# Kernel optimization log

Measured on AMD Instinct MI355X. Metric: run time of the kernel, lower is better.

## Reference

```python
import jax, jax.numpy as jnp
import numpy as np

H, HD, D = 16, 64, 1024
SCALE = HD ** -0.5
TEMP = 1.0
EPS = 1e-5

def setup_inputs() -> dict:
    key = jax.random.key(0)
    ks = jax.random.split(key, 10)
    B, N = 2, 2048
    lim = 1.0 / np.sqrt(D)
    def lin(k, out_d, in_d):
        k1, k2 = jax.random.split(k)
        W = jax.random.uniform(k1, (out_d, in_d), jnp.float32, -lim, lim)
        b = jax.random.uniform(k2, (out_d,), jnp.float32, -lim, lim)
        return W, b
    Wq, bq = lin(ks[0], H * HD, D)
    Wk, bk = lin(ks[1], H * HD, D)
    Wv, bv = lin(ks[2], H * HD, D)
    Wo, bo = lin(ks[3], D, H * HD)
    return {
        "x": jax.random.normal(ks[4], (B, N, D), jnp.float32),
        "adaptive_scale": jnp.ones((H,), jnp.float32),
        "Wq": Wq, "bq": bq, "Wk": Wk, "bk": bk, "Wv": Wv, "bv": bv,
        "Wo": Wo, "bo": bo,
        "gamma": jnp.ones((D,), jnp.float32),
        "beta": jnp.zeros((D,), jnp.float32),
    }

def reference(x, adaptive_scale, Wq, bq, Wk, bk, Wv, bv, Wo, bo, gamma, beta):
    B, N, _ = x.shape
    # self-attention: context = x
    Q = (x @ Wq.T + bq).reshape(B, N, H, HD)
    K = (x @ Wk.T + bk).reshape(B, N, H, HD)
    V = (x @ Wv.T + bv).reshape(B, N, H, HD)
    # per-head adaptive scale folded into scores (matches naive QK^T * scale / temp)
    scores = jnp.einsum('bnhd,bmhd->bhnm', Q, K)
    scores = scores * (SCALE * adaptive_scale)[None, :, None, None] / TEMP
    w = jax.nn.softmax(scores, axis=-1)  # [B,H,N,N]
    attn = jnp.einsum('bhnm,bmhd->bnhd', w, V).reshape(B, N, H * HD)
    y = x + (attn @ Wo.T + bo)
    mu = jnp.mean(y, axis=-1, keepdims=True)
    var = jnp.var(y, axis=-1, keepdims=True)
    return (y - mu) / jnp.sqrt(var + EPS) * gamma + beta
```

## Files before the change

### kernel.cpp

```cpp
#include <hip/hip_runtime.h>
#include <hip/hip_bf16.h>

using bf16 = __hip_bfloat16;
typedef __attribute__((ext_vector_type(8))) short short8;
typedef __attribute__((ext_vector_type(4))) float f32x4;

#define MFMA16(a, b, c) __builtin_amdgcn_mfma_f32_16x16x32_bf16((a), (b), (c), 0, 0, 0)

__device__ inline void async16(bf16* lds, const bf16* g) {
  __builtin_amdgcn_global_load_lds(
      (const __attribute__((address_space(1))) void*)g,
      (__attribute__((address_space(3))) void*)lds, 16, 0, 0);
}

__global__ __launch_bounds__(256) void cvt_all(
    const float* __restrict__ x,  const float* __restrict__ Wq,
    const float* __restrict__ Wk, const float* __restrict__ Wv,
    const float* __restrict__ Wo,
    bf16* __restrict__ xb, bf16* __restrict__ Wqb, bf16* __restrict__ Wkb,
    bf16* __restrict__ Wvb, bf16* __restrict__ Wob) {
  int i = blockIdx.x * 256 + threadIdx.x;
  const float* s; bf16* d; int off;
  if (i < 1048576)      { s = x;  d = xb;  off = i; }
  else if (i < 1310720) { s = Wq; d = Wqb; off = i - 1048576; }
  else if (i < 1572864) { s = Wk; d = Wkb; off = i - 1310720; }
  else if (i < 1835008) { s = Wv; d = Wvb; off = i - 1572864; }
  else                  { s = Wo; d = Wob; off = i - 1835008; }
  float4 v = ((const float4*)s)[off];
  struct __align__(8) B4 { bf16 a, b, c, d; };
  B4 o{__float2bfloat16(v.x), __float2bfloat16(v.y),
       __float2bfloat16(v.z), __float2bfloat16(v.w)};
  *(B4*)&d[(size_t)off * 4] = o;
}

__global__ __launch_bounds__(256) void gemm_qkv(
    const bf16* __restrict__ A,
    const bf16* __restrict__ Wq, const bf16* __restrict__ Wk, const bf16* __restrict__ Wv,
    const float* __restrict__ bq, const float* __restrict__ bk, const float* __restrict__ bv,
    const float* __restrict__ asc,
    bf16* __restrict__ Qb, bf16* __restrict__ Kb, bf16* __restrict__ Vtb) {
  __shared__ __align__(16) bf16 As[128 * 32];
  __shared__ __align__(16) bf16 Bs[128 * 32];

  const int tid = threadIdx.x;
  const int lane = tid & 63;
  const int w = tid >> 6;
  const int m0 = blockIdx.x * 128;
  const int region = blockIdx.y >> 3;
  const int n0loc = (blockIdx.y & 7) * 128;
  const int wm = (w >> 1) * 64;
  const int wn = (w & 1) * 64;
  const int rq = lane & 15;
  const int quad = lane >> 4;
  const int kq = quad * 8;

  const bf16* W = region == 0 ? Wq : (region == 1 ? Wk : Wv);
  const float* bias = region == 0 ? bq : (region == 1 ? bk : bv);
  bf16* C = region == 0 ? Qb : (region == 1 ? Kb : Vtb);

  f32x4 acc[4][4] = {};
  const bf16* Ag = A + (size_t)m0 * 1024;
  const bf16* Wg = W + (size_t)n0loc * 1024;

  for (int k0 = 0; k0 < 1024; k0 += 32) {
    __syncthreads();
#pragma unroll
    for (int rep = 0; rep < 2; ++rep) {
      int c = tid + rep * 256;
      int row = c >> 2;
      int ce = (c & 3) * 8;
      async16(&As[c * 8], Ag + (size_t)row * 1024 + k0 + ce);
      async16(&Bs[c * 8], Wg + (size_t)row * 1024 + k0 + ce);
    }
    __syncthreads();

    short8 a[4], b[4];
#pragma unroll
    for (int i = 0; i < 4; ++i) a[i] = *(const short8*)&As[(wm + i * 16 + rq) * 32 + kq];
#pragma unroll
    for (int j = 0; j < 4; ++j) b[j] = *(const short8*)&Bs[(wn + j * 16 + rq) * 32 + kq];
#pragma unroll
    for (int i = 0; i < 4; ++i)
#pragma unroll
      for (int j = 0; j < 4; ++j) acc[i][j] = MFMA16(a[i], b[j], acc[i][j]);
  }

  const float LOG2E = 1.44269504088896f;
#pragma unroll
  for (int i = 0; i < 4; ++i)
#pragma unroll
    for (int j = 0; j < 4; ++j)
#pragma unroll
      for (int r2 = 0; r2 < 4; ++r2) {
        int m = m0 + wm + i * 16 + quad * 4 + r2;
        int nr = n0loc + wn + j * 16 + rq;
        int bb = m >> 11, t = m & 2047, h = nr >> 6, hd = nr & 63;
        float v = acc[i][j][r2] + bias[nr];
        if (region == 0) v *= 0.125f * asc[h] * LOG2E;
        bf16 ov = __float2bfloat16(v);
        if (region < 2)
          C[(((size_t)(bb * 16 + h)) * 2048 + t) * 64 + hd] = ov;
        else
          C[(((size_t)(bb * 16 + h)) * 64 + hd) * 2048 + t] = ov;
      }
}

__global__ __launch_bounds__(256) void gemm_out(
    const bf16* __restrict__ A, const bf16* __restrict__ W,
    const float* __restrict__ bias, const float* __restrict__ R,
    float* __restrict__ Y) {
  __shared__ __align__(16) bf16 As[128 * 32];
  __shared__ __align__(16) bf16 Bs[128 * 32];

  const int tid = threadIdx.x;
  const int lane = tid & 63;
  const int w = tid >> 6;
  const int m0 = blockIdx.x * 128;
  const int n0 = blockIdx.y * 128;
  const int wm = (w >> 1) * 64;
  const int wn = (w & 1) * 64;
  const int rq = lane & 15;
  const int quad = lane >> 4;
  const int kq = quad * 8;

  f32x4 acc[4][4] = {};
  const bf16* Ag = A + (size_t)m0 * 1024;
  const bf16* Wg = W + (size_t)n0 * 1024;

  for (int k0 = 0; k0 < 1024; k0 += 32) {
    __syncthreads();
#pragma unroll
    for (int rep = 0; rep < 2; ++rep) {
      int c = tid + rep * 256;
      int row = c >> 2;
      int ce = (c & 3) * 8;
      async16(&As[c * 8], Ag + (size_t)row * 1024 + k0 + ce);
      async16(&Bs[c * 8], Wg + (size_t)row * 1024 + k0 + ce);
    }
    __syncthreads();

    short8 a[4], b[4];
#pragma unroll
    for (int i = 0; i < 4; ++i) a[i] = *(const short8*)&As[(wm + i * 16 + rq) * 32 + kq];
#pragma unroll
    for (int j = 0; j < 4; ++j) b[j] = *(const short8*)&Bs[(wn + j * 16 + rq) * 32 + kq];
#pragma unroll
    for (int i = 0; i < 4; ++i)
#pragma unroll
      for (int j = 0; j < 4; ++j) acc[i][j] = MFMA16(a[i], b[j], acc[i][j]);
  }

#pragma unroll
  for (int i = 0; i < 4; ++i)
#pragma unroll
    for (int j = 0; j < 4; ++j)
#pragma unroll
      for (int r2 = 0; r2 < 4; ++r2) {
        int m = m0 + wm + i * 16 + quad * 4 + r2;
        int n = n0 + wn + j * 16 + rq;
        Y[(size_t)m * 1024 + n] = acc[i][j][r2] + bias[n] + R[(size_t)m * 1024 + n];
      }
}

#define LP 72
__global__ __launch_bounds__(256, 3) void attn_kernel(
    const bf16* __restrict__ Qb, const bf16* __restrict__ Kb,
    const bf16* __restrict__ Vtb,
    bf16* __restrict__ P0, bf16* __restrict__ P1, float* __restrict__ lbuf) {
  __shared__ __align__(16) bf16 Ks[64 * 64];
  __shared__ __align__(16) bf16 Vs[64 * 64];
  __shared__ __align__(16) bf16 Ps[4][32 * LP];

  const int q0 = blockIdx.x * 128;
  const int h = blockIdx.y;
  const int b = blockIdx.z & 1;
  const int half = blockIdx.z >> 1;
  const int tid = threadIdx.x;
  const int lane = tid & 63;
  const int w = tid >> 6;
  const int rq = lane & 15;
  const int quad = lane >> 4;
  const int kq = quad * 8;

  const size_t head = ((size_t)(b * 16 + h)) * 2048 * 64;
  const bf16* Qh = Qb + head;
  const bf16* Kh = Kb + head;
  const bf16* Vh = Vtb + head;

  short8 aq[2][2];
#pragma unroll
  for (int s = 0; s < 2; ++s) {
    const bf16* qrow = Qh + (size_t)(q0 + w * 32 + s * 16 + rq) * 64;
    aq[s][0] = *(const short8*)&qrow[kq];
    aq[s][1] = *(const short8*)&qrow[kq + 32];
  }

  short8 ones;
#pragma unroll
  for (int i = 0; i < 8; ++i) ones[i] = (short)0x3F80;

  const int srow = lane >> 3;
  const int sws = ((lane & 7) ^ srow) * 8;
  const int c0 = (quad ^ (rq & 7)) * 8;
  const int c1 = c0 ^ 32;

  f32x4 accO[2][4] = {};
  f32x4 lacc[2] = {};

  const int kt0 = half * 16;
  for (int kt = kt0; kt < kt0 + 16; ++kt) {
    __syncthreads();
#pragma unroll
    for (int t = 0; t < 2; ++t) {
      int rb = w * 16 + t * 8;
      int row = rb + srow;
      async16(&Ks[rb * 64 + lane * 8], Kh + (size_t)(kt * 64 + row) * 64 + sws);
      async16(&Vs[rb * 64 + lane * 8], Vh + (size_t)row * 2048 + kt * 64 + sws);
    }
    __syncthreads();

    f32x4 S[2][4] = {};
#pragma unroll
    for (int j = 0; j < 4; ++j) {
      short8 bk0 = *(const short8*)&Ks[(j * 16 + rq) * 64 + c0];
      short8 bk1 = *(const short8*)&Ks[(j * 16 + rq) * 64 + c1];
      S[0][j] = MFMA16(aq[0][0], bk0, S[0][j]);
      S[0][j] = MFMA16(aq[0][1], bk1, S[0][j]);
      S[1][j] = MFMA16(aq[1][0], bk0, S[1][j]);
      S[1][j] = MFMA16(aq[1][1], bk1, S[1][j]);
    }

#pragma unroll
    for (int s = 0; s < 2; ++s)
#pragma unroll
      for (int r = 0; r < 4; ++r)
#pragma unroll
        for (int j = 0; j < 4; ++j)
          Ps[w][(s * 16 + quad * 4 + r) * LP + j * 16 + rq] =
              __float2bfloat16(exp2f(S[s][j][r]));

    short8 ap[2][2];
#pragma unroll
    for (int s = 0; s < 2; ++s) {
      ap[s][0] = *(const short8*)&Ps[w][(s * 16 + rq) * LP + kq];
      ap[s][1] = *(const short8*)&Ps[w][(s * 16 + rq) * LP + kq + 32];
    }

#pragma unroll
    for (int dt = 0; dt < 4; ++dt) {
      short8 bv0 = *(const short8*)&Vs[(dt * 16 + rq) * 64 + c0];
      short8 bv1 = *(const short8*)&Vs[(dt * 16 + rq) * 64 + c1];
#pragma unroll
      for (int s = 0; s < 2; ++s) {
        accO[s][dt] = MFMA16(ap[s][0], bv0, accO[s][dt]);
        accO[s][dt] = MFMA16(ap[s][1], bv1, accO[s][dt]);
      }
    }
#pragma unroll
    for (int s = 0; s < 2; ++s) {
      lacc[s] = MFMA16(ap[s][0], ones, lacc[s]);
      lacc[s] = MFMA16(ap[s][1], ones, lacc[s]);
    }
  }

  bf16* Pout = half ? P1 : P0;
  float* lout = lbuf + half * 65536;
#pragma unroll
  for (int s = 0; s < 2; ++s) {
#pragma unroll
    for (int dt = 0; dt < 4; ++dt)
#pragma unroll
      for (int r = 0; r < 4; ++r) {
        int t = q0 + w * 32 + s * 16 + quad * 4 + r;
        int d = dt * 16 + rq;
        Pout[((size_t)(b * 2048 + t)) * 1024 + h * 64 + d] =
            __float2bfloat16(accO[s][dt][r]);
      }
    if (rq == 0) {
#pragma unroll
      for (int r = 0; r < 4; ++r) {
        int t = q0 + w * 32 + s * 16 + quad * 4 + r;
        lout[(b * 16 + h) * 2048 + t] = lacc[s][r];
      }
    }
  }
}

__global__ __launch_bounds__(256) void combine_kernel(
    bf16* __restrict__ P0, const bf16* __restrict__ P1,
    const float* __restrict__ lbuf) {
  const int row = blockIdx.x;
  const int tid = threadIdx.x;
  const int col = tid * 4;
  const int b = row >> 11, t = row & 2047;
  const int h = col >> 6;
  const float l = lbuf[(b * 16 + h) * 2048 + t] + lbuf[65536 + (b * 16 + h) * 2048 + t];
  const float rl = 1.f / l;
  size_t base = (size_t)row * 1024 + col;
  struct __align__(8) B4 { bf16 a, b, c, d; };
  B4 p0 = *(const B4*)&P0[base];
  B4 p1 = *(const B4*)&P1[base];
  B4 o;
  o.a = __float2bfloat16((__bfloat162float(p0.a) + __bfloat162float(p1.a)) * rl);
  o.b = __float2bfloat16((__bfloat162float(p0.b) + __bfloat162float(p1.b)) * rl);
  o.c = __float2bfloat16((__bfloat162float(p0.c) + __bfloat162float(p1.c)) * rl);
  o.d = __float2bfloat16((__bfloat162float(p0.d) + __bfloat162float(p1.d)) * rl);
  *(B4*)&P0[base] = o;
}

__global__ __launch_bounds__(256) void ln_kernel(
    const float* __restrict__ Y, const float* __restrict__ gamma,
    const float* __restrict__ beta, float* __restrict__ out) {
  const int row = blockIdx.x;
  const int tid = threadIdx.x;
  const int lane = tid & 63;
  const int w = tid >> 6;
  const float* y = Y + (size_t)row * 1024;

  float4 v = *(const float4*)&y[tid * 4];
  float s = v.x + v.y + v.z + v.w;
  float ss = v.x * v.x + v.y * v.y + v.z * v.z + v.w * v.w;
#pragma unroll
  for (int msk = 1; msk < 64; msk <<= 1) {
    s += __shfl_xor(s, msk);
    ss += __shfl_xor(ss, msk);
  }
  __shared__ float red[2][4];
  if (lane == 0) { red[0][w] = s; red[1][w] = ss; }
  __syncthreads();
  s = red[0][0] + red[0][1] + red[0][2] + red[0][3];
  ss = red[1][0] + red[1][1] + red[1][2] + red[1][3];
  float mean = s * (1.f / 1024.f);
  float var = ss * (1.f / 1024.f) - mean * mean;
  float rstd = rsqrtf(var + 1e-5f);
  float4 g = *(const float4*)&gamma[tid * 4];
  float4 bt = *(const float4*)&beta[tid * 4];
  float4 o;
  o.x = (v.x - mean) * rstd * g.x + bt.x;
  o.y = (v.y - mean) * rstd * g.y + bt.y;
  o.z = (v.z - mean) * rstd * g.z + bt.z;
  o.w = (v.w - mean) * rstd * g.w + bt.w;
  *(float4*)&out[(size_t)row * 1024 + tid * 4] = o;
}

extern "C" void kernel_launch(void* const* d_in, const int* in_sizes, int n_in,
                              void* d_out, int out_size, void* d_ws, size_t ws_size,
                              hipStream_t stream) {
  const float* x     = (const float*)d_in[0];
  const float* asc   = (const float*)d_in[1];
  const float* Wq    = (const float*)d_in[2];
  const float* bq    = (const float*)d_in[3];
  const float* Wk    = (const float*)d_in[4];
  const float* bk    = (const float*)d_in[5];
  const float* Wv    = (const float*)d_in[6];
  const float* bv    = (const float*)d_in[7];
  const float* Wo    = (const float*)d_in[8];
  const float* bo    = (const float*)d_in[9];
  const float* gamma = (const float*)d_in[10];
  const float* beta  = (const float*)d_in[11];
  float* out = (float*)d_out;

  char* ws = (char*)d_ws;
  const size_t MB = 1024 * 1024;
  bf16* Qb   = (bf16*)(ws);
  bf16* Kb   = (bf16*)(ws + 8 * MB);
  bf16* Vtb  = (bf16*)(ws + 16 * MB);
  bf16* attn = (bf16*)(ws + 24 * MB);
  bf16* xb   = (bf16*)(ws + 32 * MB);
  bf16* Wqb  = (bf16*)(ws + 40 * MB);
  bf16* Wkb  = (bf16*)(ws + 42 * MB);
  bf16* Wvb  = (bf16*)(ws + 44 * MB);
  bf16* Wob  = (bf16*)(ws + 46 * MB);
  float* y   = (float*)(ws);
  bf16* P1   = xb;
  float* lbuf = (float*)Wqb;

  dim3 bb(256);

  cvt_all<<<dim3(8192), bb, 0, stream>>>(x, Wq, Wk, Wv, Wo, xb, Wqb, Wkb, Wvb, Wob);
  gemm_qkv<<<dim3(32, 24), bb, 0, stream>>>(xb, Wqb, Wkb, Wvb, bq, bk, bv, asc, Qb, Kb, Vtb);
  attn_kernel<<<dim3(16, 16, 4), bb, 0, stream>>>(Qb, Kb, Vtb, attn, P1, lbuf);
  combine_kernel<<<dim3(4096), bb, 0, stream>>>(attn, P1, lbuf);
  gemm_out<<<dim3(32, 8), bb, 0, stream>>>(attn, Wob, bo, x, y);
  ln_kernel<<<dim3(4096), bb, 0, stream>>>(y, gamma, beta, out);
}
```

Baseline: 240.6 us.

## Double attention query tile per wave, vectorize P stores, transpose V via LDS

The attention kernel now gives each wave 64 query rows instead of 32, with 256-row blocks, so K/V tiles loaded into LDS are reused across twice as many queries. K fragments are loaded once per tile in a permuted key order, which lets each lane write four exp'd probabilities as one packed 8-byte LDS store. The V-transpose epilogue of the QKV GEMM is staged through a per-wave LDS scratch so global writes are 4-element vectors along the token axis instead of scattered 2-byte stores. Small packing helpers vectorize the cvt and combine kernels. The price is higher register pressure and occupancy lowered to 2 blocks per SU, with half as many attention blocks.

```diff
diff --git a/kernel.cpp b/kernel.cpp
--- a/kernel.cpp
+++ b/kernel.cpp
@@ -3,6 +3,7 @@
 
 using bf16 = __hip_bfloat16;
 typedef __attribute__((ext_vector_type(8))) short short8;
+typedef __attribute__((ext_vector_type(4))) short short4v;
 typedef __attribute__((ext_vector_type(4))) float f32x4;
 
 #define MFMA16(a, b, c) __builtin_amdgcn_mfma_f32_16x16x32_bf16((a), (b), (c), 0, 0, 0)
@@ -11,6 +12,13 @@
   __builtin_amdgcn_global_load_lds(
       (const __attribute__((address_space(1))) void*)g,
       (__attribute__((address_space(3))) void*)lds, 16, 0, 0);
+}
+
+__device__ inline short bfs(float x) {
+  union { bf16 h; short s; } u; u.h = __float2bfloat16(x); return u.s;
+}
+__device__ inline short4v pack4(float a, float b, float c, float d) {
+  short4v r; r[0] = bfs(a); r[1] = bfs(b); r[2] = bfs(c); r[3] = bfs(d); return r;
 }
 
 __global__ __launch_bounds__(256) void cvt_all(
@@ -27,10 +35,8 @@
   else if (i < 1835008) { s = Wv; d = Wvb; off = i - 1572864; }
   else                  { s = Wo; d = Wob; off = i - 1835008; }
   float4 v = ((const float4*)s)[off];
-  struct __align__(8) B4 { bf16 a, b, c, d; };
-  B4 o{__float2bfloat16(v.x), __float2bfloat16(v.y),
-       __float2bfloat16(v.z), __float2bfloat16(v.w)};
-  *(B4*)&d[(size_t)off * 4] = o;
+  short4v o = pack4(v.x, v.y, v.z, v.w);
+  *(short4v*)&d[(size_t)off * 4] = o;
 }
 
 __global__ __launch_bounds__(256) void gemm_qkv(
@@ -41,6 +47,7 @@
     bf16* __restrict__ Qb, bf16* __restrict__ Kb, bf16* __restrict__ Vtb) {
   __shared__ __align__(16) bf16 As[128 * 32];
   __shared__ __align__(16) bf16 Bs[128 * 32];
+  __shared__ __align__(16) bf16 scrT[4][16 * 68];
 
   const int tid = threadIdx.x;
   const int lane = tid & 63;
@@ -86,23 +93,44 @@
   }
 
   const float LOG2E = 1.44269504088896f;
-#pragma unroll
-  for (int i = 0; i < 4; ++i)
-#pragma unroll
-    for (int j = 0; j < 4; ++j)
-#pragma unroll
-      for (int r2 = 0; r2 < 4; ++r2) {
-        int m = m0 + wm + i * 16 + quad * 4 + r2;
-        int nr = n0loc + wn + j * 16 + rq;
-        int bb = m >> 11, t = m & 2047, h = nr >> 6, hd = nr & 63;
-        float v = acc[i][j][r2] + bias[nr];
-        if (region == 0) v *= 0.125f * asc[h] * LOG2E;
-        bf16 ov = __float2bfloat16(v);
-        if (region < 2)
-          C[(((size_t)(bb * 16 + h)) * 2048 + t) * 64 + hd] = ov;
-        else
-          C[(((size_t)(bb * 16 + h)) * 64 + hd) * 2048 + t] = ov;
-      }
+  if (region < 2) {
+#pragma unroll
+    for (int i = 0; i < 4; ++i)
+#pragma unroll
+      for (int j = 0; j < 4; ++j)
+#pragma unroll
+        for (int r2 = 0; r2 < 4; ++r2) {
+          int m = m0 + wm + i * 16 + quad * 4 + r2;
+          int nr = n0loc + wn + j * 16 + rq;
+          int bb = m >> 11, t = m & 2047, h = nr >> 6, hd = nr & 63;
+          float v = acc[i][j][r2] + bias[nr];
+          if (region == 0) v *= 0.125f * asc[h] * LOG2E;
+          C[(((size_t)(bb * 16 + h)) * 2048 + t) * 64 + hd] = __float2bfloat16(v);
+        }
+  } else {
+    const int bb = m0 >> 11;
+    const int h = (n0loc + wn) >> 6;
+    const int tbase = (m0 & 2047) + wm;
+    bf16* scr = scrT[w];
+#pragma unroll
+    for (int j = 0; j < 4; ++j) {
+      int nr = n0loc + wn + j * 16 + rq;
+      float bi = bias[nr];
+#pragma unroll
+      for (int i = 0; i < 4; ++i) {
+        short4v pv = pack4(acc[i][j][0] + bi, acc[i][j][1] + bi,
+                           acc[i][j][2] + bi, acc[i][j][3] + bi);
+        *(short4v*)&scr[rq * 68 + i * 16 + quad * 4] = pv;
+      }
+#pragma unroll
+      for (int pp = 0; pp < 4; ++pp) {
+        int hdl = pp * 4 + quad;
+        short4v v4 = *(const short4v*)&scr[hdl * 68 + rq * 4];
+        size_t addr = (((size_t)(bb * 16 + h)) * 64 + j * 16 + hdl) * 2048 + tbase + rq * 4;
+        *(short4v*)&C[addr] = v4;
+      }
+    }
+  }
 }
 
 __global__ __launch_bounds__(256) void gemm_out(
@@ -163,15 +191,15 @@
 }
 
 #define LP 72
-__global__ __launch_bounds__(256, 3) void attn_kernel(
+__global__ __launch_bounds__(256, 2) void attn_kernel(
     const bf16* __restrict__ Qb, const bf16* __restrict__ Kb,
     const bf16* __restrict__ Vtb,
     bf16* __restrict__ P0, bf16* __restrict__ P1, float* __restrict__ lbuf) {
   __shared__ __align__(16) bf16 Ks[64 * 64];
   __shared__ __align__(16) bf16 Vs[64 * 64];
-  __shared__ __align__(16) bf16 Ps[4][32 * LP];
-
-  const int q0 = blockIdx.x * 128;
+  __shared__ __align__(16) bf16 Ps[4][64 * LP];
+
+  const int q0 = blockIdx.x * 256;
   const int h = blockIdx.y;
   const int b = blockIdx.z & 1;
   const int half = blockIdx.z >> 1;
@@ -187,10 +215,10 @@
   const bf16* Kh = Kb + head;
   const bf16* Vh = Vtb + head;
 
-  short8 aq[2][2];
-#pragma unroll
-  for (int s = 0; s < 2; ++s) {
-    const bf16* qrow = Qh + (size_t)(q0 + w * 32 + s * 16 + rq) * 64;
+  short8 aq[4][2];
+#pragma unroll
+  for (int s = 0; s < 4; ++s) {
+    const bf16* qrow = Qh + (size_t)(q0 + w * 64 + s * 16 + rq) * 64;
     aq[s][0] = *(const short8*)&qrow[kq];
     aq[s][1] = *(const short8*)&qrow[kq + 32];
   }
@@ -204,8 +232,8 @@
   const int c0 = (quad ^ (rq & 7)) * 8;
   const int c1 = c0 ^ 32;
 
-  f32x4 accO[2][4] = {};
-  f32x4 lacc[2] = {};
+  f32x4 accO[4][4] = {};
+  f32x4 lacc[4] = {};
 
   const int kt0 = half * 16;
   for (int kt = kt0; kt < kt0 + 16; ++kt) {
@@ -219,59 +247,61 @@
     }
     __syncthreads();
 
-    f32x4 S[2][4] = {};
+    short8 bk[4][2];
 #pragma unroll
     for (int j = 0; j < 4; ++j) {
-      short8 bk0 = *(const short8*)&Ks[(j * 16 + rq) * 64 + c0];
-      short8 bk1 = *(const short8*)&Ks[(j * 16 + rq) * 64 + c1];
-      S[0][j] = MFMA16(aq[0][0], bk0, S[0][j]);
-      S[0][j] = MFMA16(aq[0][1], bk1, S[0][j]);
-      S[1][j] = MFMA16(aq[1][0], bk0, S[1][j]);
-      S[1][j] = MFMA16(aq[1][1], bk1, S[1][j]);
-    }
-
-#pragma unroll
-    for (int s = 0; s < 2; ++s)
-#pragma unroll
-      for (int r = 0; r < 4; ++r)
-#pragma unroll
-        for (int j = 0; j < 4; ++j)
-          Ps[w][(s * 16 + quad * 4 + r) * LP + j * 16 + rq] =
-              __float2bfloat16(exp2f(S[s][j][r]));
-
-    short8 ap[2][2];
-#pragma unroll
-    for (int s = 0; s < 2; ++s) {
-      ap[s][0] = *(const short8*)&Ps[w][(s * 16 + rq) * LP + kq];
-      ap[s][1] = *(const short8*)&Ps[w][(s * 16 + rq) * LP + kq + 32];
-    }
-
+      int sw = (quad ^ ((4 * (rq & 1) + j) & 7)) * 8;
+      const bf16* kr = &Ks[(rq * 4 + j) * 64];
+      bk[j][0] = *(const short8*)&kr[sw];
+      bk[j][1] = *(const short8*)&kr[sw ^ 32];
+    }
+
+#pragma unroll
+    for (int s = 0; s < 4; ++s) {
+      f32x4 S[4] = {};
+#pragma unroll
+      for (int j = 0; j < 4; ++j) {
+        S[j] = MFMA16(aq[s][0], bk[j][0], S[j]);
+        S[j] = MFMA16(aq[s][1], bk[j][1], S[j]);
+      }
+#pragma unroll
+      for (int r = 0; r < 4; ++r) {
+        short4v pv = pack4(exp2f(S[0][r]), exp2f(S[1][r]),
+                           exp2f(S[2][r]), exp2f(S[3][r]));
+        *(short4v*)&Ps[w][(s * 16 + quad * 4 + r) * LP + rq * 4] = pv;
+      }
+    }
+
+    short8 bv[4][2];
 #pragma unroll
     for (int dt = 0; dt < 4; ++dt) {
-      short8 bv0 = *(const short8*)&Vs[(dt * 16 + rq) * 64 + c0];
-      short8 bv1 = *(const short8*)&Vs[(dt * 16 + rq) * 64 + c1];
-#pragma unroll
-      for (int s = 0; s < 2; ++s) {
-        accO[s][dt] = MFMA16(ap[s][0], bv0, accO[s][dt]);
-        accO[s][dt] = MFMA16(ap[s][1], bv1, accO[s][dt]);
-      }
-    }
-#pragma unroll
-    for (int s = 0; s < 2; ++s) {
-      lacc[s] = MFMA16(ap[s][0], ones, lacc[s]);
-      lacc[s] = MFMA16(ap[s][1], ones, lacc[s]);
+      const bf16* vr = &Vs[(dt * 16 + rq) * 64];
+      bv[dt][0] = *(const short8*)&vr[c0];
+      bv[dt][1] = *(const short8*)&vr[c1];
+    }
+#pragma unroll
+    for (int s = 0; s < 4; ++s) {
+      short8 ap0 = *(const short8*)&Ps[w][(s * 16 + rq) * LP + kq];
+      short8 ap1 = *(const short8*)&Ps[w][(s * 16 + rq) * LP + kq + 32];
+#pragma unroll
+      for (int dt = 0; dt < 4; ++dt) {
+        accO[s][dt] = MFMA16(ap0, bv[dt][0], accO[s][dt]);
+        accO[s][dt] = MFMA16(ap1, bv[dt][1], accO[s][dt]);
+      }
+      lacc[s] = MFMA16(ap0, ones, lacc[s]);
+      lacc[s] = MFMA16(ap1, ones, lacc[s]);
     }
   }
 
   bf16* Pout = half ? P1 : P0;
   float* lout = lbuf + half * 65536;
 #pragma unroll
-  for (int s = 0; s < 2; ++s) {
+  for (int s = 0; s < 4; ++s) {
 #pragma unroll
     for (int dt = 0; dt < 4; ++dt)
 #pragma unroll
       for (int r = 0; r < 4; ++r) {
-        int t = q0 + w * 32 + s * 16 + quad * 4 + r;
+        int t = q0 + w * 64 + s * 16 + quad * 4 + r;
         int d = dt * 16 + rq;
         Pout[((size_t)(b * 2048 + t)) * 1024 + h * 64 + d] =
             __float2bfloat16(accO[s][dt][r]);
@@ -279,7 +309,7 @@
     if (rq == 0) {
 #pragma unroll
       for (int r = 0; r < 4; ++r) {
-        int t = q0 + w * 32 + s * 16 + quad * 4 + r;
+        int t = q0 + w * 64 + s * 16 + quad * 4 + r;
         lout[(b * 16 + h) * 2048 + t] = lacc[s][r];
       }
     }
@@ -297,15 +327,17 @@
   const float l = lbuf[(b * 16 + h) * 2048 + t] + lbuf[65536 + (b * 16 + h) * 2048 + t];
   const float rl = 1.f / l;
   size_t base = (size_t)row * 1024 + col;
-  struct __align__(8) B4 { bf16 a, b, c, d; };
-  B4 p0 = *(const B4*)&P0[base];
-  B4 p1 = *(const B4*)&P1[base];
-  B4 o;
-  o.a = __float2bfloat16((__bfloat162float(p0.a) + __bfloat162float(p1.a)) * rl);
-  o.b = __float2bfloat16((__bfloat162float(p0.b) + __bfloat162float(p1.b)) * rl);
-  o.c = __float2bfloat16((__bfloat162float(p0.c) + __bfloat162float(p1.c)) * rl);
-  o.d = __float2bfloat16((__bfloat162float(p0.d) + __bfloat162float(p1.d)) * rl);
-  *(B4*)&P0[base] = o;
+  short4v p0 = *(const short4v*)&P0[base];
+  short4v p1 = *(const short4v*)&P1[base];
+  union { short s; bf16 h; } u;
+  float v[4];
+#pragma unroll
+  for (int i = 0; i < 4; ++i) {
+    u.s = p0[i]; float a = __bfloat162float(u.h);
+    u.s = p1[i]; float c = __bfloat162float(u.h);
+    v[i] = (a + c) * rl;
+  }
+  *(short4v*)&P0[base] = pack4(v[0], v[1], v[2], v[3]);
 }
 
 __global__ __launch_bounds__(256) void ln_kernel(
@@ -379,7 +411,7 @@
 
   cvt_all<<<dim3(8192), bb, 0, stream>>>(x, Wq, Wk, Wv, Wo, xb, Wqb, Wkb, Wvb, Wob);
   gemm_qkv<<<dim3(32, 24), bb, 0, stream>>>(xb, Wqb, Wkb, Wvb, bq, bk, bv, asc, Qb, Kb, Vtb);
-  attn_kernel<<<dim3(16, 16, 4), bb, 0, stream>>>(Qb, Kb, Vtb, attn, P1, lbuf);
+  attn_kernel<<<dim3(8, 16, 4), bb, 0, stream>>>(Qb, Kb, Vtb, attn, P1, lbuf);
   combine_kernel<<<dim3(4096), bb, 0, stream>>>(attn, P1, lbuf);
   gemm_out<<<dim3(32, 8), bb, 0, stream>>>(attn, Wob, bo, x, y);
   ln_kernel<<<dim3(4096), bb, 0, stream>>>(y, gamma, beta, out);
```

Measured after the change: 226.3 us. 1.06x faster.
